# Optimization experiments

Hardware: AMD Instinct MI355X
Metric: run time of the kernel (lower is better)

The kernel has to match this reference:

```python
import jax, jax.numpy as jnp
import numpy as np

NUM_HEADS = 12
EPS = 1e-6


def setup_inputs() -> dict:
    key = jax.random.key(0)
    k1, k2, k3, k4 = jax.random.split(key, 4)
    N, B, D = 1025, 8, 768
    x = jax.random.normal(k1, (N, B, D), dtype=jnp.float32)
    # torch nn.Linear weights: [out_features, in_features]
    w_qkv = jax.random.normal(k2, (3 * D, D), dtype=jnp.float32) * (D ** -0.5)
    w_proj = jax.random.normal(k3, (D, D), dtype=jnp.float32) * (D ** -0.5)
    b_proj = jax.random.normal(k4, (D,), dtype=jnp.float32) * 0.01
    return {"x": x, "w_qkv": w_qkv, "w_proj": w_proj, "b_proj": b_proj}


def reference(x, w_qkv, w_proj, b_proj):
    N, B, D = x.shape
    H = NUM_HEADS
    hd = D // H
    scale = hd ** -0.5
    scale_vv = scale * 1.0  # scale_multiplier = 1.0

    xb = jnp.transpose(x, (1, 0, 2))  # [B, N, D]
    qkv = xb @ w_qkv.T  # [B, N, 3D]
    qkv = qkv.reshape(B, N, 3, H, hd).transpose(2, 0, 3, 1, 4)  # [3, B, H, N, hd]
    q, k, v = qkv[0], qkv[1], qkv[2]

    # QK path: only row 0 of out_ori survives the masking, compute just that row
    scores0 = jnp.einsum('bhqd,bhkd->bhqk', q[:, :, :1], k) * scale  # [B,H,1,N]
    attn0 = jax.nn.softmax(scores0, axis=-1)
    out0 = jnp.einsum('bhqk,bhkd->bhqd', attn0, v)  # [B,H,1,hd]

    # VV cosine path: only rows 1: survive
    vn = v / jnp.maximum(jnp.linalg.norm(v, axis=-1, keepdims=True), EPS)
    scores_vv = jnp.einsum('bhqd,bhkd->bhqk', vn[:, :, 1:], vn) * scale_vv  # [B,H,N-1,N]
    attn_vv = jax.nn.softmax(scores_vv, axis=-1)
    out_vv = jnp.einsum('bhqk,bhkd->bhqd', attn_vv, v)  # [B,H,N-1,hd]

    out = jnp.concatenate([out0, out_vv], axis=2)  # [B,H,N,hd]
    out = out.transpose(0, 2, 1, 3).reshape(B, N, D)
    out = out @ w_proj.T + b_proj
    return jnp.transpose(out, (1, 0, 2))  # [N, B, D]
```

## Files before the change

### kernel.cpp

```cpp
#include <hip/hip_runtime.h>

typedef unsigned short u16;
typedef unsigned int   u32;
typedef __attribute__((ext_vector_type(8))) short short8;
typedef __attribute__((ext_vector_type(4))) float f32x4;

#define AS1 __attribute__((address_space(1)))
#define AS3 __attribute__((address_space(3)))

#define NSEQ  1025
#define BB    8
#define DD    768
#define HH    12
#define MROWS 8200
#define MPAD  8320
#define KPAD  1088

__device__ __forceinline__ void gl2lds16(const void* g, void* l) {
  __builtin_amdgcn_global_load_lds((const AS1 u32*)g, (AS3 u32*)l, 16, 0, 0);
}
__device__ __forceinline__ u16 f2bf(float f) {
  u32 u = __float_as_uint(f);
  return (u16)((u + 0x7FFFu + ((u >> 16) & 1u)) >> 16);
}
__device__ __forceinline__ float bf2f(u16 u) { return __uint_as_float(((u32)u) << 16); }

__global__ __launch_bounds__(256) void prep(const float* __restrict__ x,
                                            const float* __restrict__ wqkv,
                                            const float* __restrict__ wproj,
                                            u16* __restrict__ xb,
                                            u16* __restrict__ wkv,
                                            u16* __restrict__ wpj,
                                            float* __restrict__ q0) {
  __shared__ float red[256];
  const int XB_G  = MPAD * 192;
  const int WKV_G = 1536 * 192;
  const int WPJ_G = 768 * 192;
  if (blockIdx.x >= 7968) {
    int bid = blockIdx.x - 7968;
    int b = bid / HH, c = bid - b * HH;
    int tid = threadIdx.x;
    int dp = (c << 6) + (tid >> 2), part = tid & 3;
    const float4* x4 = (const float4*)(x + (size_t)b * DD + part * 192);
    const float4* w4 = (const float4*)(wqkv + (size_t)dp * DD + part * 192);
    float acc = 0.f;
#pragma unroll 4
    for (int e = 0; e < 48; ++e) {
      float4 a = x4[e], w = w4[e];
      acc += a.x * w.x + a.y * w.y + a.z * w.z + a.w * w.w;
    }
    red[tid] = acc;
    __syncthreads();
    if (part == 0) q0[b * DD + dp] = red[tid] + red[tid + 1] + red[tid + 2] + red[tid + 3];
    return;
  }
  int g = blockIdx.x * 256 + threadIdx.x;
  float4 v;
  u16* dst;
  size_t di;
  if (g < XB_G) {
    int m = g / 192, e4 = g - m * 192;
    if (m < MROWS) {
      int bb = m / NSEQ, ns = m - bb * NSEQ;
      v = ((const float4*)x)[(size_t)(ns * BB + bb) * 192 + e4];
    } else {
      v.x = v.y = v.z = v.w = 0.f;
    }
    dst = xb; di = (size_t)g;
  } else if (g < XB_G + WKV_G) {
    int r = g - XB_G;
    v = ((const float4*)wqkv)[(size_t)147456 + r];
    dst = wkv; di = (size_t)r;
  } else if (g < XB_G + WKV_G + WPJ_G) {
    int r = g - XB_G - WKV_G;
    v = ((const float4*)wproj)[r];
    dst = wpj; di = (size_t)r;
  } else {
    return;
  }
  uint2 o;
  o.x = (u32)f2bf(v.x) | ((u32)f2bf(v.y) << 16);
  o.y = (u32)f2bf(v.z) | ((u32)f2bf(v.w) << 16);
  ((uint2*)dst)[di] = o;
}

template <int MODE, int NT>
__global__ __launch_bounds__(256) void gemm_bt(const u16* __restrict__ A,
                                               const u16* __restrict__ W,
                                               u16* __restrict__ Cbf,
                                               float* __restrict__ Cf,
                                               const float* __restrict__ bias,
                                               int ldc) {
  __shared__ u16 sA[128 * 64];
  __shared__ u16 sW[128 * 64];
  const int id = blockIdx.x;
  const int rx = id & 7, qx = id >> 3;
  const int kq = qx / NT;
  const int m_t = rx + (kq << 3);
  if (m_t > 64) return;
  const int n_t = qx - kq * NT;
  const int m0 = m_t << 7, n0 = n_t << 7;

  const int tid = threadIdx.x;
  const int w = tid >> 6, lane = tid & 63;
  const int wm = w & 1, wn = w >> 1;
  const int lc = lane & 15, lr = lane >> 4;

  f32x4 zero4 = {0.f, 0.f, 0.f, 0.f};
  f32x4 acc[4][4];
#pragma unroll
  for (int i = 0; i < 4; ++i)
#pragma unroll
    for (int j = 0; j < 4; ++j) acc[i][j] = zero4;

  const int r0 = tid >> 3;
  const int ko = (tid & 7) << 3;
  const u16* gA = A + (size_t)(m0 + r0) * DD + ko;
  const u16* gW = W + (size_t)(n0 + r0) * DD + ko;
  char* lA = (char*)sA + tid * 16;
  char* lW = (char*)sW + tid * 16;

#pragma unroll 1
  for (int kt = 0; kt < 12; ++kt) {
    __syncthreads();
#pragma unroll
    for (int j = 0; j < 4; ++j) {
      gl2lds16(gA + (size_t)j * 32 * DD + kt * 64, lA + j * 4096);
      gl2lds16(gW + (size_t)j * 32 * DD + kt * 64, lW + j * 4096);
    }
    __syncthreads();
#pragma unroll
    for (int kk = 0; kk < 2; ++kk) {
      short8 af[4], wf[4];
#pragma unroll
      for (int mt = 0; mt < 4; ++mt)
        af[mt] = *(const short8*)((char*)sA + ((wm << 6) + (mt << 4) + lc) * 128 + (kk << 6) + (lr << 4));
#pragma unroll
      for (int nt = 0; nt < 4; ++nt)
        wf[nt] = *(const short8*)((char*)sW + ((wn << 6) + (nt << 4) + lc) * 128 + (kk << 6) + (lr << 4));
#pragma unroll
      for (int mt = 0; mt < 4; ++mt)
#pragma unroll
        for (int nt = 0; nt < 4; ++nt)
          acc[mt][nt] = __builtin_amdgcn_mfma_f32_16x16x32_bf16(af[mt], wf[nt], acc[mt][nt], 0, 0, 0);
    }
  }

  if (MODE == 0) {
#pragma unroll
    for (int mt = 0; mt < 4; ++mt)
#pragma unroll
      for (int r = 0; r < 4; ++r) {
        int m = m0 + (wm << 6) + (mt << 4) + (lr << 2) + r;
        if (m < MROWS) {
          size_t base = (size_t)m * ldc + n0 + (wn << 6) + lc;
#pragma unroll
          for (int nt = 0; nt < 4; ++nt) Cbf[base + (nt << 4)] = f2bf(acc[mt][nt][r]);
        }
      }
  } else {
    float b4[4];
#pragma unroll
    for (int nt = 0; nt < 4; ++nt) b4[nt] = bias[n0 + (wn << 6) + (nt << 4) + lc];
#pragma unroll
    for (int mt = 0; mt < 4; ++mt)
#pragma unroll
      for (int r = 0; r < 4; ++r) {
        int m = m0 + (wm << 6) + (mt << 4) + (lr << 2) + r;
        if (m < MROWS) {
          int bb = m / NSEQ;
          int ns = m - bb * NSEQ;
          float* o = Cf + (size_t)ns * (BB * DD) + bb * DD + n0 + (wn << 6) + lc;
#pragma unroll
          for (int nt = 0; nt < 4; ++nt) o[nt << 4] = acc[mt][nt][r] + b4[nt];
        }
      }
  }
}

__global__ __launch_bounds__(256) void transpose_v(const u16* __restrict__ kv,
                                                   u16* __restrict__ vT,
                                                   u16* __restrict__ vn) {
  __shared__ u16 tile[64][72];
  __shared__ float red[256];
  __shared__ float sInv[64];
  int bid = blockIdx.x;
  int kc = bid % 17;
  int t2 = bid / 17;
  int h = t2 % HH, b = t2 / HH;
  int tid = threadIdx.x;
  int kl = tid >> 2, dc = (tid & 3) << 4;
  int key = kc * 64 + kl;
  u32 vals[8];
  if (key < NSEQ) {
    const u32* g = (const u32*)(kv + ((size_t)b * NSEQ + key) * 1536 + DD + h * 64 + dc);
#pragma unroll
    for (int i = 0; i < 8; ++i) vals[i] = g[i];
  } else {
#pragma unroll
    for (int i = 0; i < 8; ++i) vals[i] = 0;
  }
  float part = 0.f;
#pragma unroll
  for (int i = 0; i < 8; ++i) {
    float a = bf2f((u16)(vals[i] & 0xFFFF));
    float c = bf2f((u16)(vals[i] >> 16));
    part += a * a + c * c;
    ((u32*)&tile[kl][dc])[i] = vals[i];
  }
  red[tid] = part;
  __syncthreads();
  if ((tid & 3) == 0) {
    float s = red[tid] + red[tid + 1] + red[tid + 2] + red[tid + 3];
    sInv[kl] = (key < NSEQ) ? 1.0f / fmaxf(sqrtf(s), 1e-6f) : 0.0f;
  }
  __syncthreads();
  float iv = sInv[kl];
  u32 ovn[8];
#pragma unroll
  for (int i = 0; i < 8; ++i) {
    float a = bf2f((u16)(vals[i] & 0xFFFF)) * iv;
    float c = bf2f((u16)(vals[i] >> 16)) * iv;
    ovn[i] = (u32)f2bf(a) | ((u32)f2bf(c) << 16);
  }
  u32* on = (u32*)(vn + ((size_t)(b * HH + h) * KPAD + key) * 64 + dc);
#pragma unroll
  for (int i = 0; i < 8; ++i) on[i] = ovn[i];
  int dl = tid >> 2, ks = (tid & 3) << 4;
  u32 ov[8];
#pragma unroll
  for (int i = 0; i < 8; ++i)
    ov[i] = (u32)tile[ks + 2 * i][dl] | ((u32)tile[ks + 2 * i + 1][dl] << 16);
  u16* o = vT + (size_t)(b * HH + h) * 64 * KPAD + (size_t)dl * KPAD + kc * 64 + ks;
#pragma unroll
  for (int i = 0; i < 8; ++i) ((u32*)o)[i] = ov[i];
}

__global__ __launch_bounds__(256) void row0_attn(const float* __restrict__ q0,
                                                 const u16* __restrict__ kv,
                                                 u16* __restrict__ attn) {
  __shared__ float sq[64];
  __shared__ float sc[NSEQ];
  __shared__ float red[256];
  __shared__ float rpv[32][68];
  int bid = blockIdx.x;
  int b = bid / HH, h = bid - b * HH;
  int tid = threadIdx.x;
  if (tid < 64) sq[tid] = q0[b * DD + h * 64 + tid];
  __syncthreads();
  float mx = -1e30f;
  for (int n = tid; n < NSEQ; n += 256) {
    const u32* kr = (const u32*)(kv + ((size_t)b * NSEQ + n) * 1536 + h * 64);
    float s = 0.f;
#pragma unroll
    for (int i = 0; i < 32; ++i) {
      u32 u = kr[i];
      s += bf2f((u16)(u & 0xFFFF)) * sq[2 * i] + bf2f((u16)(u >> 16)) * sq[2 * i + 1];
    }
    s *= 0.125f;
    sc[n] = s;
    mx = fmaxf(mx, s);
  }
  red[tid] = mx;
  __syncthreads();
  for (int st = 128; st > 0; st >>= 1) {
    if (tid < st) red[tid] = fmaxf(red[tid], red[tid + st]);
    __syncthreads();
  }
  mx = red[0];
  __syncthreads();
  float ds = 0.f;
  for (int n = tid; n < NSEQ; n += 256) {
    float p = __expf(sc[n] - mx);
    sc[n] = p;
    ds += p;
  }
  red[tid] = ds;
  __syncthreads();
  for (int st = 128; st > 0; st >>= 1) {
    if (tid < st) red[tid] += red[tid + st];
    __syncthreads();
  }
  float den = red[0];
  __syncthreads();

  int kp = tid >> 3, dc = (tid & 7) << 3;
  const u16* vb = kv + (size_t)b * NSEQ * 1536 + DD + h * 64 + dc;
  float acc[8];
#pragma unroll
  for (int i = 0; i < 8; ++i) acc[i] = 0.f;
#pragma unroll 4
  for (int j = 0; j < 32; ++j) {
    int n = kp + (j << 5);
    uint4 v = *(const uint4*)(vb + (size_t)n * 1536);
    float p = sc[n];
    acc[0] += p * bf2f((u16)(v.x & 0xFFFF));
    acc[1] += p * bf2f((u16)(v.x >> 16));
    acc[2] += p * bf2f((u16)(v.y & 0xFFFF));
    acc[3] += p * bf2f((u16)(v.y >> 16));
    acc[4] += p * bf2f((u16)(v.z & 0xFFFF));
    acc[5] += p * bf2f((u16)(v.z >> 16));
    acc[6] += p * bf2f((u16)(v.w & 0xFFFF));
    acc[7] += p * bf2f((u16)(v.w >> 16));
  }
  if (kp == 0) {
    uint4 v = *(const uint4*)(vb + (size_t)1024 * 1536);
    float p = sc[1024];
    acc[0] += p * bf2f((u16)(v.x & 0xFFFF));
    acc[1] += p * bf2f((u16)(v.x >> 16));
    acc[2] += p * bf2f((u16)(v.y & 0xFFFF));
    acc[3] += p * bf2f((u16)(v.y >> 16));
    acc[4] += p * bf2f((u16)(v.z & 0xFFFF));
    acc[5] += p * bf2f((u16)(v.z >> 16));
    acc[6] += p * bf2f((u16)(v.w & 0xFFFF));
    acc[7] += p * bf2f((u16)(v.w >> 16));
  }
#pragma unroll
  for (int i = 0; i < 8; ++i) rpv[kp][dc + i] = acc[i];
  __syncthreads();
  if (tid < 64) {
    float s = 0.f;
#pragma unroll
    for (int p = 0; p < 32; ++p) s += rpv[p][tid];
    attn[(size_t)b * NSEQ * DD + h * 64 + tid] = f2bf(s / den);
  }
}

__global__ __launch_bounds__(256, 4) void vv_attn(const u16* __restrict__ vn,
                                                  const u16* __restrict__ vT,
                                                  u16* __restrict__ attn) {
  __shared__ u16 sK[2][4096];
  __shared__ u16 sV[2][4096];
  __shared__ u16 sP[4096];

  const int tid = threadIdx.x, w = tid >> 6, lane = tid & 63;
  const int lc = lane & 15, lr = lane >> 4;
  const int bh = blockIdx.x;
  const int m0 = blockIdx.y << 7;
  const int b = bh / HH, h = bh - b * HH;
  const char* nb = (const char*)(vn + (size_t)bh * KPAD * 64);
  const char* tb = (const char*)(vT + (size_t)bh * 64 * KPAD);

  short8 qreg[2][2];
#pragma unroll
  for (int kk = 0; kk < 2; ++kk)
#pragma unroll
    for (int nt = 0; nt < 2; ++nt)
      qreg[kk][nt] = *(const short8*)(nb +
          (size_t)(1 + m0 + (w << 5) + (nt << 4) + lc) * 128 + (kk << 6) + (lr << 4));

  const char* srcK[2];
  const char* srcV[2];
  int offKV[2];
#pragma unroll
  for (int j = 0; j < 2; ++j) {
    int lin = (w << 11) + (j << 10) + (lane << 4);
    int kk = lin >> 12, kg = (lin >> 10) & 3;
    int lr2 = (lin >> 8) & 3, lc2 = (lin >> 4) & 15;
    srcK[j] = nb + (size_t)((kg << 4) + lc2) * 128 + (kk << 6) + (lr2 << 4);
    srcV[j] = tb + (size_t)((kg << 4) + lc2) * (KPAD * 2) + (kk << 6) + (lr2 << 4);
    offKV[j] = lin;
  }

  f32x4 zero4 = {0.f, 0.f, 0.f, 0.f};
  f32x4 oacc[2][4];
  f32x4 dacc[2];
#pragma unroll
  for (int i = 0; i < 2; ++i) {
    dacc[i] = zero4;
#pragma unroll
    for (int j = 0; j < 4; ++j) oacc[i][j] = zero4;
  }
  short8 ones;
#pragma unroll
  for (int i = 0; i < 8; ++i) ones[i] = (short)0x3F80;

  const float CEXP = 0.1803368801111204f;

  const char* rdP = (const char*)sP + (w << 11) + (lane << 4);
  char* wrP = (char*)sP + (w << 11) + ((lr >> 1) << 8) + (lc << 4) + ((lr & 1) << 3);

#pragma unroll
  for (int j = 0; j < 2; ++j) {
    gl2lds16(srcK[j], (char*)sK + offKV[j]);
    gl2lds16(srcV[j], (char*)sV + offKV[j]);
  }

#pragma unroll 1
  for (int kt = 0; kt < 17; ++kt) {
    const int cur = kt & 1;
    __syncthreads();
    if (kt < 16) {
#pragma unroll
      for (int j = 0; j < 2; ++j) {
        gl2lds16(srcK[j] + (size_t)(kt + 1) * 8192, (char*)sK + (cur ^ 1) * 8192 + offKV[j]);
        gl2lds16(srcV[j] + (size_t)(kt + 1) * 128,  (char*)sV + (cur ^ 1) * 8192 + offKV[j]);
      }
    }
    const char* rdK = (const char*)sK + cur * 8192 + (lane << 4);
    const char* rdV = (const char*)sV + cur * 8192 + (lane << 4);

    f32x4 sacc[4][2];
#pragma unroll
    for (int mt = 0; mt < 4; ++mt)
#pragma unroll
      for (int nt = 0; nt < 2; ++nt) sacc[mt][nt] = zero4;
#pragma unroll
    for (int kk = 0; kk < 2; ++kk) {
      short8 ak[4];
#pragma unroll
      for (int mt = 0; mt < 4; ++mt)
        ak[mt] = *(const short8*)(rdK + (kk << 12) + (mt << 10));
#pragma unroll
      for (int mt = 0; mt < 4; ++mt)
#pragma unroll
        for (int nt = 0; nt < 2; ++nt)
          sacc[mt][nt] = __builtin_amdgcn_mfma_f32_16x16x32_bf16(ak[mt], qreg[kk][nt], sacc[mt][nt], 0, 0, 0);
    }

#pragma unroll
    for (int h2 = 0; h2 < 2; ++h2) {
      if (!(kt == 16 && h2 == 1)) {
        asm volatile("" ::: "memory");
#pragma unroll
        for (int mi = 0; mi < 2; ++mi) {
          int ms = (h2 << 1) + mi;
#pragma unroll
          for (int nt = 0; nt < 2; ++nt) {
            f32x4 s = sacc[ms][nt];
            u32 a0 = __float_as_uint(__builtin_amdgcn_exp2f(s[0] * CEXP)) + 0x8000u;
            u32 a1 = __float_as_uint(__builtin_amdgcn_exp2f(s[1] * CEXP)) + 0x8000u;
            u32 a2 = __float_as_uint(__builtin_amdgcn_exp2f(s[2] * CEXP)) + 0x8000u;
            u32 a3 = __float_as_uint(__builtin_amdgcn_exp2f(s[3] * CEXP)) + 0x8000u;
            uint2 pv;
            pv.x = __builtin_amdgcn_perm(a1, a0, 0x07060302u);
            pv.y = __builtin_amdgcn_perm(a3, a2, 0x07060302u);
            if (kt == 16) {
              pv.x = (ms == 0 && lr == 0) ? (pv.x & 0xFFFFu) : 0u;
              pv.y = 0u;
            }
            *(uint2*)(wrP + (nt << 10) + (mi << 9)) = pv;
          }
        }
        __builtin_amdgcn_sched_barrier(0);
        asm volatile("" ::: "memory");
        short8 ap[2], bv[4];
#pragma unroll
        for (int mt = 0; mt < 2; ++mt)
          ap[mt] = *(const short8*)(rdP + (mt << 10));
#pragma unroll
        for (int nt = 0; nt < 4; ++nt)
          bv[nt] = *(const short8*)(rdV + (h2 << 12) + (nt << 10));
#pragma unroll
        for (int mt = 0; mt < 2; ++mt) {
#pragma unroll
          for (int nt = 0; nt < 4; ++nt)
            oacc[mt][nt] = __builtin_amdgcn_mfma_f32_16x16x32_bf16(ap[mt], bv[nt], oacc[mt][nt], 0, 0, 0);
          dacc[mt] = __builtin_amdgcn_mfma_f32_16x16x32_bf16(ap[mt], ones, dacc[mt], 0, 0, 0);
        }
      }
    }
  }

#pragma unroll
  for (int mt = 0; mt < 2; ++mt) {
#pragma unroll
    for (int r = 0; r < 4; ++r) {
      int q = (w << 5) + (mt << 4) + (lr << 2) + r;
      int nseq = 1 + m0 + q;
      float rdn = 1.0f / dacc[mt][r];
      size_t obase = ((size_t)b * NSEQ + nseq) * DD + h * 64 + lc;
#pragma unroll
      for (int nt = 0; nt < 4; ++nt) attn[obase + (nt << 4)] = f2bf(oacc[mt][nt][r] * rdn);
    }
  }
}

extern "C" void kernel_launch(void* const* d_in, const int* in_sizes, int n_in,
                              void* d_out, int out_size, void* d_ws, size_t ws_size,
                              hipStream_t stream) {
  const float* x      = (const float*)d_in[0];
  const float* w_qkv  = (const float*)d_in[1];
  const float* w_proj = (const float*)d_in[2];
  const float* b_proj = (const float*)d_in[3];
  float* out = (float*)d_out;
  char* ws = (char*)d_ws;

  u16*   xb   = (u16*)(ws + 0);
  u16*   vT   = (u16*)(ws + 0);
  u16*   wkv  = (u16*)(ws + 13369344);
  u16*   wpj  = (u16*)(ws + 15728640);
  u16*   kvb  = (u16*)(ws + 16908288);
  float* q0   = (float*)(ws + 42467328);
  u16*   attn = (u16*)(ws + 42491904);
  u16*   vn   = (u16*)(ws + 55271424);

  prep<<<8064, 256, 0, stream>>>(x, w_qkv, w_proj, xb, wkv, wpj, q0);
  gemm_bt<0, 12><<<864, 256, 0, stream>>>(xb, wkv, kvb, nullptr, nullptr, 1536);
  transpose_v<<<1632, 256, 0, stream>>>(kvb, vT, vn);
  row0_attn<<<96, 256, 0, stream>>>(q0, kvb, attn);
  vv_attn<<<dim3(96, 8), 256, 0, stream>>>(vn, vT, attn);
  gemm_bt<1, 6><<<432, 256, 0, stream>>>(attn, wpj, nullptr, out, b_proj, 768);
}
```

Baseline: 235.7 us.

## Split row-0 attention across key chunks and drop vv_attn LDS double buffering

Row-0 attention now runs as 8 key-chunk blocks per (batch, head) and writes unnormalized partial numerators and denominators. vv_attn combines these partials at the end, which removes the max subtraction in row-0 (exp of raw scores). The q0 matvec moves out of prep into its own kernel launched after the QKV GEMM, adding one launch. vv_attn also drops K/V double buffering in favour of single-buffered loads with two barriers per tile, and computes all exp values before the PV MFMAs. That exposes load latency in exchange for less LDS and possibly higher occupancy.

```diff
diff --git a/kernel.cpp b/kernel.cpp
--- a/kernel.cpp
+++ b/kernel.cpp
@@ -30,30 +30,10 @@
                                             const float* __restrict__ wproj,
                                             u16* __restrict__ xb,
                                             u16* __restrict__ wkv,
-                                            u16* __restrict__ wpj,
-                                            float* __restrict__ q0) {
-  __shared__ float red[256];
+                                            u16* __restrict__ wpj) {
   const int XB_G  = MPAD * 192;
   const int WKV_G = 1536 * 192;
   const int WPJ_G = 768 * 192;
-  if (blockIdx.x >= 7968) {
-    int bid = blockIdx.x - 7968;
-    int b = bid / HH, c = bid - b * HH;
-    int tid = threadIdx.x;
-    int dp = (c << 6) + (tid >> 2), part = tid & 3;
-    const float4* x4 = (const float4*)(x + (size_t)b * DD + part * 192);
-    const float4* w4 = (const float4*)(wqkv + (size_t)dp * DD + part * 192);
-    float acc = 0.f;
-#pragma unroll 4
-    for (int e = 0; e < 48; ++e) {
-      float4 a = x4[e], w = w4[e];
-      acc += a.x * w.x + a.y * w.y + a.z * w.z + a.w * w.w;
-    }
-    red[tid] = acc;
-    __syncthreads();
-    if (part == 0) q0[b * DD + dp] = red[tid] + red[tid + 1] + red[tid + 2] + red[tid + 3];
-    return;
-  }
   int g = blockIdx.x * 256 + threadIdx.x;
   float4 v;
   u16* dst;
@@ -178,6 +158,27 @@
   }
 }
 
+__global__ __launch_bounds__(256) void q0_kernel(const float* __restrict__ x,
+                                                 const float* __restrict__ wq,
+                                                 float* __restrict__ q0) {
+  __shared__ float red[256];
+  int bid = blockIdx.x;
+  int b = bid / HH, c = bid - b * HH;
+  int tid = threadIdx.x;
+  int dp = (c << 6) + (tid >> 2), part = tid & 3;
+  const float4* x4 = (const float4*)(x + (size_t)b * DD + part * 192);
+  const float4* w4 = (const float4*)(wq + (size_t)dp * DD + part * 192);
+  float acc = 0.f;
+#pragma unroll 4
+  for (int e = 0; e < 48; ++e) {
+    float4 a = x4[e], w = w4[e];
+    acc += a.x * w.x + a.y * w.y + a.z * w.z + a.w * w.w;
+  }
+  red[tid] = acc;
+  __syncthreads();
+  if (part == 0) q0[b * DD + dp] = red[tid] + red[tid + 1] + red[tid + 2] + red[tid + 3];
+}
+
 __global__ __launch_bounds__(256) void transpose_v(const u16* __restrict__ kv,
                                                    u16* __restrict__ vT,
                                                    u16* __restrict__ vn) {
@@ -236,20 +237,22 @@
   for (int i = 0; i < 8; ++i) ((u32*)o)[i] = ov[i];
 }
 
-__global__ __launch_bounds__(256) void row0_attn(const float* __restrict__ q0,
+__global__ __launch_bounds__(256) void row0_part(const float* __restrict__ q0,
                                                  const u16* __restrict__ kv,
-                                                 u16* __restrict__ attn) {
+                                                 float* __restrict__ part) {
   __shared__ float sq[64];
-  __shared__ float sc[NSEQ];
+  __shared__ float sc[129];
   __shared__ float red[256];
   __shared__ float rpv[32][68];
-  int bid = blockIdx.x;
-  int b = bid / HH, h = bid - b * HH;
+  int bh = blockIdx.x, ck = blockIdx.y;
+  int b = bh / HH, h = bh - b * HH;
   int tid = threadIdx.x;
   if (tid < 64) sq[tid] = q0[b * DD + h * 64 + tid];
-  __syncthreads();
-  float mx = -1e30f;
-  for (int n = tid; n < NSEQ; n += 256) {
+  if (tid == 64) sc[128] = 0.f;
+  __syncthreads();
+  const int nk = (ck == 7) ? 129 : 128;
+  if (tid < nk) {
+    int n = ck * 128 + tid;
     const u32* kr = (const u32*)(kv + ((size_t)b * NSEQ + n) * 1536 + h * 64);
     float s = 0.f;
 #pragma unroll
@@ -257,43 +260,26 @@
       u32 u = kr[i];
       s += bf2f((u16)(u & 0xFFFF)) * sq[2 * i] + bf2f((u16)(u >> 16)) * sq[2 * i + 1];
     }
-    s *= 0.125f;
-    sc[n] = s;
-    mx = fmaxf(mx, s);
-  }
-  red[tid] = mx;
-  __syncthreads();
-  for (int st = 128; st > 0; st >>= 1) {
-    if (tid < st) red[tid] = fmaxf(red[tid], red[tid + st]);
-    __syncthreads();
-  }
-  mx = red[0];
-  __syncthreads();
-  float ds = 0.f;
-  for (int n = tid; n < NSEQ; n += 256) {
-    float p = __expf(sc[n] - mx);
-    sc[n] = p;
-    ds += p;
-  }
+    sc[tid] = __expf(s * 0.125f);
+  }
+  __syncthreads();
+  float ds = (tid < nk) ? sc[tid] : 0.f;
   red[tid] = ds;
   __syncthreads();
   for (int st = 128; st > 0; st >>= 1) {
     if (tid < st) red[tid] += red[tid + st];
     __syncthreads();
   }
-  float den = red[0];
-  __syncthreads();
-
   int kp = tid >> 3, dc = (tid & 7) << 3;
   const u16* vb = kv + (size_t)b * NSEQ * 1536 + DD + h * 64 + dc;
   float acc[8];
 #pragma unroll
   for (int i = 0; i < 8; ++i) acc[i] = 0.f;
-#pragma unroll 4
-  for (int j = 0; j < 32; ++j) {
-    int n = kp + (j << 5);
-    uint4 v = *(const uint4*)(vb + (size_t)n * 1536);
-    float p = sc[n];
+#pragma unroll
+  for (int j = 0; j < 4; ++j) {
+    int kl = kp + (j << 5);
+    uint4 v = *(const uint4*)(vb + (size_t)(ck * 128 + kl) * 1536);
+    float p = sc[kl];
     acc[0] += p * bf2f((u16)(v.x & 0xFFFF));
     acc[1] += p * bf2f((u16)(v.x >> 16));
     acc[2] += p * bf2f((u16)(v.y & 0xFFFF));
@@ -303,9 +289,9 @@
     acc[6] += p * bf2f((u16)(v.w & 0xFFFF));
     acc[7] += p * bf2f((u16)(v.w >> 16));
   }
-  if (kp == 0) {
+  if (ck == 7 && kp == 0) {
     uint4 v = *(const uint4*)(vb + (size_t)1024 * 1536);
-    float p = sc[1024];
+    float p = sc[128];
     acc[0] += p * bf2f((u16)(v.x & 0xFFFF));
     acc[1] += p * bf2f((u16)(v.x >> 16));
     acc[2] += p * bf2f((u16)(v.y & 0xFFFF));
@@ -318,20 +304,23 @@
 #pragma unroll
   for (int i = 0; i < 8; ++i) rpv[kp][dc + i] = acc[i];
   __syncthreads();
+  float* po = part + ((size_t)bh * 8 + ck) * 65;
   if (tid < 64) {
     float s = 0.f;
 #pragma unroll
     for (int p = 0; p < 32; ++p) s += rpv[p][tid];
-    attn[(size_t)b * NSEQ * DD + h * 64 + tid] = f2bf(s / den);
-  }
+    po[tid] = s;
+  }
+  if (tid == 64) po[64] = red[0];
 }
 
 __global__ __launch_bounds__(256, 4) void vv_attn(const u16* __restrict__ vn,
                                                   const u16* __restrict__ vT,
-                                                  u16* __restrict__ attn) {
-  __shared__ u16 sK[2][4096];
-  __shared__ u16 sV[2][4096];
-  __shared__ u16 sP[4096];
+                                                  u16* __restrict__ attn,
+                                                  const float* __restrict__ part) {
+  __shared__ u16 sK[4096];
+  __shared__ u16 sV[4096];
+  __shared__ u16 sP[8192];
 
   const int tid = threadIdx.x, w = tid >> 6, lane = tid & 63;
   const int lc = lane & 15, lr = lane >> 4;
@@ -377,28 +366,20 @@
 
   const float CEXP = 0.1803368801111204f;
 
-  const char* rdP = (const char*)sP + (w << 11) + (lane << 4);
-  char* wrP = (char*)sP + (w << 11) + ((lr >> 1) << 8) + (lc << 4) + ((lr & 1) << 3);
-
-#pragma unroll
-  for (int j = 0; j < 2; ++j) {
-    gl2lds16(srcK[j], (char*)sK + offKV[j]);
-    gl2lds16(srcV[j], (char*)sV + offKV[j]);
-  }
+  const char* rdK = (const char*)sK + (lane << 4);
+  const char* rdV = (const char*)sV + (lane << 4);
+  const char* rdP = (const char*)sP + (w << 12) + (lane << 4);
+  char* wrP = (char*)sP + (w << 12) + ((lr >> 1) << 8) + (lc << 4) + ((lr & 1) << 3);
 
 #pragma unroll 1
   for (int kt = 0; kt < 17; ++kt) {
-    const int cur = kt & 1;
     __syncthreads();
-    if (kt < 16) {
-#pragma unroll
-      for (int j = 0; j < 2; ++j) {
-        gl2lds16(srcK[j] + (size_t)(kt + 1) * 8192, (char*)sK + (cur ^ 1) * 8192 + offKV[j]);
-        gl2lds16(srcV[j] + (size_t)(kt + 1) * 128,  (char*)sV + (cur ^ 1) * 8192 + offKV[j]);
-      }
-    }
-    const char* rdK = (const char*)sK + cur * 8192 + (lane << 4);
-    const char* rdV = (const char*)sV + cur * 8192 + (lane << 4);
+#pragma unroll
+    for (int j = 0; j < 2; ++j) {
+      gl2lds16(srcK[j] + (size_t)kt * 8192, (char*)sK + offKV[j]);
+      gl2lds16(srcV[j] + (size_t)kt * 128,  (char*)sV + offKV[j]);
+    }
+    __syncthreads();
 
     f32x4 sacc[4][2];
 #pragma unroll
@@ -419,35 +400,34 @@
     }
 
 #pragma unroll
+    for (int mt = 0; mt < 4; ++mt) {
+#pragma unroll
+      for (int nt = 0; nt < 2; ++nt) {
+        f32x4 s = sacc[mt][nt];
+        u32 a0 = __float_as_uint(__builtin_amdgcn_exp2f(s[0] * CEXP)) + 0x8000u;
+        u32 a1 = __float_as_uint(__builtin_amdgcn_exp2f(s[1] * CEXP)) + 0x8000u;
+        u32 a2 = __float_as_uint(__builtin_amdgcn_exp2f(s[2] * CEXP)) + 0x8000u;
+        u32 a3 = __float_as_uint(__builtin_amdgcn_exp2f(s[3] * CEXP)) + 0x8000u;
+        uint2 pv;
+        pv.x = __builtin_amdgcn_perm(a1, a0, 0x07060302u);
+        pv.y = __builtin_amdgcn_perm(a3, a2, 0x07060302u);
+        if (kt == 16) {
+          pv.x = (mt == 0 && lr == 0) ? (pv.x & 0xFFFFu) : 0u;
+          pv.y = 0u;
+        }
+        *(uint2*)(wrP + ((mt >> 1) << 11) + (nt << 10) + ((mt & 1) << 9)) = pv;
+      }
+    }
+    __builtin_amdgcn_sched_barrier(0);
+    asm volatile("" ::: "memory");
+
+#pragma unroll
     for (int h2 = 0; h2 < 2; ++h2) {
       if (!(kt == 16 && h2 == 1)) {
-        asm volatile("" ::: "memory");
-#pragma unroll
-        for (int mi = 0; mi < 2; ++mi) {
-          int ms = (h2 << 1) + mi;
-#pragma unroll
-          for (int nt = 0; nt < 2; ++nt) {
-            f32x4 s = sacc[ms][nt];
-            u32 a0 = __float_as_uint(__builtin_amdgcn_exp2f(s[0] * CEXP)) + 0x8000u;
-            u32 a1 = __float_as_uint(__builtin_amdgcn_exp2f(s[1] * CEXP)) + 0x8000u;
-            u32 a2 = __float_as_uint(__builtin_amdgcn_exp2f(s[2] * CEXP)) + 0x8000u;
-            u32 a3 = __float_as_uint(__builtin_amdgcn_exp2f(s[3] * CEXP)) + 0x8000u;
-            uint2 pv;
-            pv.x = __builtin_amdgcn_perm(a1, a0, 0x07060302u);
-            pv.y = __builtin_amdgcn_perm(a3, a2, 0x07060302u);
-            if (kt == 16) {
-              pv.x = (ms == 0 && lr == 0) ? (pv.x & 0xFFFFu) : 0u;
-              pv.y = 0u;
-            }
-            *(uint2*)(wrP + (nt << 10) + (mi << 9)) = pv;
-          }
-        }
-        __builtin_amdgcn_sched_barrier(0);
-        asm volatile("" ::: "memory");
         short8 ap[2], bv[4];
 #pragma unroll
         for (int mt = 0; mt < 2; ++mt)
-          ap[mt] = *(const short8*)(rdP + (mt << 10));
+          ap[mt] = *(const short8*)(rdP + (h2 << 11) + (mt << 10));
 #pragma unroll
         for (int nt = 0; nt < 4; ++nt)
           bv[nt] = *(const short8*)(rdV + (h2 << 12) + (nt << 10));
@@ -473,6 +453,17 @@
 #pragma unroll
       for (int nt = 0; nt < 4; ++nt) attn[obase + (nt << 4)] = f2bf(oacc[mt][nt][r] * rdn);
     }
+  }
+
+  if (blockIdx.y == 0 && tid < 64) {
+    const float* pp = part + (size_t)bh * 8 * 65;
+    float num = 0.f, den = 0.f;
+#pragma unroll
+    for (int c = 0; c < 8; ++c) {
+      num += pp[c * 65 + tid];
+      den += pp[c * 65 + 64];
+    }
+    attn[(size_t)b * NSEQ * DD + h * 64 + tid] = f2bf(num / den);
   }
 }
 
@@ -489,16 +480,18 @@
   u16*   xb   = (u16*)(ws + 0);
   u16*   vT   = (u16*)(ws + 0);
   u16*   wkv  = (u16*)(ws + 13369344);
+  float* r0p  = (float*)(ws + 13369344);
   u16*   wpj  = (u16*)(ws + 15728640);
   u16*   kvb  = (u16*)(ws + 16908288);
   float* q0   = (float*)(ws + 42467328);
   u16*   attn = (u16*)(ws + 42491904);
   u16*   vn   = (u16*)(ws + 55271424);
 
-  prep<<<8064, 256, 0, stream>>>(x, w_qkv, w_proj, xb, wkv, wpj, q0);
+  prep<<<7968, 256, 0, stream>>>(x, w_qkv, w_proj, xb, wkv, wpj);
   gemm_bt<0, 12><<<864, 256, 0, stream>>>(xb, wkv, kvb, nullptr, nullptr, 1536);
+  q0_kernel<<<96, 256, 0, stream>>>(x, w_qkv, q0);
   transpose_v<<<1632, 256, 0, stream>>>(kvb, vT, vn);
-  row0_attn<<<96, 256, 0, stream>>>(q0, kvb, attn);
-  vv_attn<<<dim3(96, 8), 256, 0, stream>>>(vn, vT, attn);
+  row0_part<<<dim3(96, 8), 256, 0, stream>>>(q0, kvb, r0p);
+  vv_attn<<<dim3(96, 8), 256, 0, stream>>>(vn, vT, attn, r0p);
   gemm_bt<1, 6><<<432, 256, 0, stream>>>(attn, wpj, nullptr, out, b_proj, 768);
 }
```

Result: faster. 214.8 us (-8.9%).
